# Kernel optimization log

Hardware: AMD Instinct MI355X
Metric: run time of the kernel (lower is better)

The kernel has to match this reference:

```python
import jax, jax.numpy as jnp
import numpy as np

S, B, D, H, DH = 2048, 2, 512, 8, 64
SCALE = 1.0 / DH ** 0.5
EPS = 1e-5
LN_EPS = 1e-5


def setup_inputs() -> dict:
    key = jax.random.key(0)
    k1, k2, k3, k4 = jax.random.split(key, 4)
    h = jax.random.normal(k1, (S, B, D), dtype=jnp.float32)
    # causal mask, True = masked out, shape [qlen, klen, 1] (dim==3 branch)
    attn_mask = jnp.triu(jnp.ones((S, S), dtype=bool), k=1)[:, :, None]
    Wq = jax.random.normal(k2, (D, H * DH), dtype=jnp.float32) * 0.02
    Wkv = jax.random.normal(k3, (D, 2 * H * DH), dtype=jnp.float32) * 0.02
    Wo = jax.random.normal(k4, (H * DH, D), dtype=jnp.float32) * 0.02
    gamma = jnp.ones((D,), dtype=jnp.float32)
    beta = jnp.zeros((D,), dtype=jnp.float32)
    return {"h": h, "Wq": Wq, "Wkv": Wkv, "Wo": Wo,
            "gamma": gamma, "beta": beta, "attn_mask": attn_mask}


def _layer_norm(x, gamma, beta):
    mu = jnp.mean(x, axis=-1, keepdims=True)
    var = jnp.mean(jnp.square(x - mu), axis=-1, keepdims=True)
    return (x - mu) * jax.lax.rsqrt(var + LN_EPS) * gamma + beta


def reference(h, Wq, Wkv, Wo, gamma, beta, attn_mask):
    # mems=None, pre_lnorm=False, dropout=dropatt=0 (eval)
    c = h
    head_q = (h @ Wq).reshape(S, B, H, DH)
    kv = (c @ Wkv)
    head_k, head_v = jnp.split(kv, 2, axis=-1)
    head_k = head_k.reshape(S, B, H, DH)
    head_v = head_v.reshape(S, B, H, DH)
    # elu(x) + 1 feature map
    head_q = jax.nn.elu(head_q) + 1.0
    head_k = jax.nn.elu(head_k) + 1.0
    # quadratic score matrix [i, j, b, n]
    attn_score = jnp.einsum('ibnd,jbnd->ijbn', head_q, head_k) * SCALE
    # dim==3 mask: [qlen, klen, 1] -> [qlen, klen, 1, 1], fill with 0
    attn_score = jnp.where(attn_mask[:, :, :, None], 0.0, attn_score)
    # sum-normalize over key axis (dim 1 = j)
    denominator = jnp.sum(attn_score, axis=1, keepdims=True) + EPS
    attn_prob = attn_score / denominator
    attn_vec = jnp.einsum('ijbn,jbnd->ibnd', attn_prob, head_v)
    attn_vec = attn_vec.reshape(S, B, H * DH)
    attn_out = attn_vec @ Wo
    # post-lnorm residual
    return _layer_norm(h + attn_out, gamma, beta)
```

## Files before the change

kernel.cpp:

```cpp
#include <hip/hip_runtime.h>
#include <hip/hip_bf16.h>
#include <math.h>

#define SCALE 0.125f
#define EPS 1e-5f
#define LN_EPS 1e-5f

typedef short short8 __attribute__((ext_vector_type(8)));
typedef float floatx4 __attribute__((ext_vector_type(4)));
typedef unsigned short us;

__device__ __forceinline__ float elu1(float x) { return x > 0.f ? x + 1.f : __expf(x); }
__device__ __forceinline__ us f2bf(float f) {
    __hip_bfloat16 b = __float2bfloat16(f);
    return __builtin_bit_cast(us, b);
}
__device__ __forceinline__ void gload_lds16(const void* g, void* lds) {
    __builtin_amdgcn_global_load_lds(
        (const __attribute__((address_space(1))) unsigned int*)g,
        (__attribute__((address_space(3))) unsigned int*)lds, 16, 0, 0);
}
__device__ __forceinline__ floatx4 mfma_bf16(short8 a, short8 b, floatx4 c) {
    return __builtin_amdgcn_mfma_f32_16x16x32_bf16(a, b, c, 0, 0, 0);
}

__global__ __launch_bounds__(256)
void pack_kernel(const float* __restrict__ h, const float* __restrict__ Wq,
                 const float* __restrict__ Wkv, const float* __restrict__ Wo,
                 us* __restrict__ hB, us* __restrict__ WqkvT, us* __restrict__ WoT,
                 us* __restrict__ VTg) {
    const int bid = blockIdx.x, tid = threadIdx.x;
    if (bid < 2048) {
        int idx = bid * 1024 + tid * 4;
        float4 v = *(const float4*)(h + idx);
        ushort4 o;
        o.x = f2bf(v.x); o.y = f2bf(v.y); o.z = f2bf(v.z); o.w = f2bf(v.w);
        *(ushort4*)(hB + idx) = o;
        return;
    }
    if (bid < 2304) {
        __shared__ us T[64][72];
        const float* src; int ld, n0s, k0; us* dst;
        if (bid < 2240) {
            int t2 = bid - 2048;
            int nt = t2 % 24, kt = t2 / 24;
            int n0 = nt * 64; k0 = kt * 64;
            if (n0 < 512) { src = Wq; ld = 512; n0s = n0; }
            else          { src = Wkv; ld = 1024; n0s = n0 - 512; }
            dst = WqkvT + (size_t)n0 * 512;
        } else {
            int t2 = bid - 2240;
            int nt = t2 & 7, kt = t2 >> 3;
            src = Wo; ld = 512; n0s = nt * 64; k0 = kt * 64;
            dst = WoT + (size_t)(nt * 64) * 512;
        }
        {
            int k = tid >> 2, cs = (tid & 3) * 16;
            const float* p = src + (size_t)(k0 + k) * ld + n0s + cs;
#pragma unroll
            for (int q = 0; q < 4; ++q) {
                float4 v = *(const float4*)(p + q * 4);
                T[k][cs + q * 4 + 0] = f2bf(v.x);
                T[k][cs + q * 4 + 1] = f2bf(v.y);
                T[k][cs + q * 4 + 2] = f2bf(v.z);
                T[k][cs + q * 4 + 3] = f2bf(v.w);
            }
        }
        __syncthreads();
        {
            int n = tid >> 2, ks = (tid & 3) * 16;
            __align__(16) us tmp[16];
#pragma unroll
            for (int j = 0; j < 16; ++j) tmp[j] = T[ks + j][n];
            us* po = dst + (size_t)n * 512 + k0 + ks;
            *(uint4*)(po) = *(uint4*)(tmp);
            *(uint4*)(po + 8) = *(uint4*)(tmp + 8);
        }
        return;
    }
    {
        int e = (bid - 2304) * 1024 + tid * 4;
        int chain = e >> 11, s = e & 2047;
        ushort4 o; o.x = 0x3f80; o.y = 0x3f80; o.z = 0x3f80; o.w = 0x3f80;
        *(ushort4*)(VTg + ((size_t)(chain * 80 + 64)) * 2048 + s) = o;
    }
}

__global__ __launch_bounds__(256)
void qkv_gemm(const us* __restrict__ A, const us* __restrict__ BT,
              us* __restrict__ Qg, us* __restrict__ Kg, us* __restrict__ VTg) {
    __shared__ __align__(16) us As[2][64 * 32];
    __shared__ __align__(16) us Bs[2][128 * 32];
    const int tid = threadIdx.x;
    const int w = tid >> 6, l = tid & 63;
    const int l15 = l & 15, l4 = l >> 4;
    const int bx = blockIdx.x;
    const int m0 = blockIdx.y * 64, n0 = bx * 128;
    const int wm = (w >> 1) * 32, wn = (w & 1) * 64;
    floatx4 acc[2][4];
#pragma unroll
    for (int i = 0; i < 2; ++i)
#pragma unroll
        for (int j = 0; j < 4; ++j)
#pragma unroll
            for (int e = 0; e < 4; ++e) acc[i][j][e] = 0.f;

    auto STAGE = [&](int buf, int kt) {
        {
            int row = w * 16 + (l >> 2);
            int g = (l & 3) ^ (row & 3);
            gload_lds16(A + (size_t)(m0 + row) * 512 + kt + g * 8, &As[buf][w * 512]);
        }
#pragma unroll
        for (int r = 0; r < 2; ++r) {
            int slot = r * 4 + w;
            int row = slot * 16 + (l >> 2);
            int g = (l & 3) ^ (row & 3);
            gload_lds16(BT + (size_t)(n0 + row) * 512 + kt + g * 8, &Bs[buf][slot * 512]);
        }
    };

    STAGE(0, 0);
    __syncthreads();
    for (int t = 0; t < 16; ++t) {
        int cur = t & 1;
        if (t < 15) STAGE(cur ^ 1, (t + 1) * 32);
        short8 a[2], b[4];
#pragma unroll
        for (int mi = 0; mi < 2; ++mi) {
            int row = wm + mi * 16 + l15;
            int p = l4 ^ (row & 3);
            a[mi] = *(const short8*)(&As[cur][row * 32 + p * 8]);
        }
#pragma unroll
        for (int ni = 0; ni < 4; ++ni) {
            int row = wn + ni * 16 + l15;
            int p = l4 ^ (row & 3);
            b[ni] = *(const short8*)(&Bs[cur][row * 32 + p * 8]);
        }
#pragma unroll
        for (int mi = 0; mi < 2; ++mi)
#pragma unroll
            for (int ni = 0; ni < 4; ++ni)
                acc[mi][ni] = mfma_bf16(a[mi], b[ni], acc[mi][ni]);
        __syncthreads();
    }
    const int region = bx >> 2;
    const int cb = (bx & 3) * 128;
    if (region < 2) {
        us* outp = region == 0 ? Qg : Kg;
#pragma unroll
        for (int mi = 0; mi < 2; ++mi)
#pragma unroll
            for (int ni = 0; ni < 4; ++ni)
#pragma unroll
                for (int r = 0; r < 4; ++r) {
                    int row = m0 + wm + mi * 16 + l4 * 4 + r;
                    int col = cb + wn + ni * 16 + l15;
                    outp[(size_t)row * 512 + col] = f2bf(elu1(acc[mi][ni][r]));
                }
    } else {
        const int hh = (bx & 3) * 2 + (w & 1);
#pragma unroll
        for (int mi = 0; mi < 2; ++mi) {
            int row0 = m0 + wm + mi * 16 + l4 * 4;
            int s0 = row0 >> 1;
#pragma unroll
            for (int ni = 0; ni < 4; ++ni) {
                int d = ni * 16 + l15;
#pragma unroll
                for (int b = 0; b < 2; ++b) {
                    unsigned int pk = (unsigned int)f2bf(acc[mi][ni][b]) |
                                      ((unsigned int)f2bf(acc[mi][ni][2 + b]) << 16);
                    *(unsigned int*)(VTg + ((size_t)((b * 8 + hh) * 80 + d)) * 2048 + s0) = pk;
                }
            }
        }
    }
}

__global__ __launch_bounds__(256)
void chunk_kv_kernel(const us* __restrict__ Kg, const us* __restrict__ VTg,
                     float* __restrict__ KVc) {
    __shared__ __align__(16) us VT_l[80 * 64];
    __shared__ __align__(16) us KT_l[64 * 72];
    const int c = blockIdx.x, chain = blockIdx.y;
    const int b = chain >> 3, hh = chain & 7;
    const int tid = threadIdx.x;
    const int w = tid >> 6, l = tid & 63;
    const int lrow = l >> 3, lg = l & 7;
#pragma unroll
    for (int r = 0; r < 3; ++r) {
        int slot = r * 4 + w;
        if (slot < 10) {
            int row = slot * 8 + lrow;
            int g = lg ^ (row & 7);
            gload_lds16(VTg + (size_t)(chain * 80 + row) * 2048 + c * 64 + g * 8,
                        VT_l + slot * 512);
        }
    }
#pragma unroll
    for (int gi = 0; gi < 2; ++gi) {
        int g = w + gi * 4;
        __align__(16) us kk[8];
#pragma unroll
        for (int e = 0; e < 8; ++e)
            kk[e] = Kg[(size_t)((c * 64 + g * 8 + e) * 2 + b) * 512 + hh * 64 + l];
        *(uint4*)(KT_l + l * 72 + g * 8) = *(uint4*)kk;
    }
    __syncthreads();
    const int l15 = l & 15, l4 = l >> 4;
    short8 af[5][2], bfr[2];
#pragma unroll
    for (int mi = 0; mi < 5; ++mi) {
        int row = mi * 16 + l15;
        int p = l4 ^ (row & 7);
        af[mi][0] = *(const short8*)(VT_l + row * 64 + p * 8);
        af[mi][1] = *(const short8*)(VT_l + row * 64 + (p ^ 4) * 8);
    }
    {
        int row = w * 16 + l15;
        bfr[0] = *(const short8*)(KT_l + row * 72 + l4 * 8);
        bfr[1] = *(const short8*)(KT_l + row * 72 + 32 + l4 * 8);
    }
    float* out = KVc + (size_t)(chain * 32 + c) * 4608;
#pragma unroll
    for (int mi = 0; mi < 5; ++mi) {
        floatx4 a = {0.f, 0.f, 0.f, 0.f};
        a = mfma_bf16(af[mi][0], bfr[0], a);
        a = mfma_bf16(af[mi][1], bfr[1], a);
#pragma unroll
        for (int r = 0; r < 4; ++r) {
            int row = mi * 16 + l4 * 4 + r;
            if (row < 65) out[row * 64 + w * 16 + l15] = a[r];
        }
    }
}

__global__ __launch_bounds__(256)
void cumsum_kernel(const float* __restrict__ KVc, us* __restrict__ MTg) {
    const int chain = blockIdx.x, rg = blockIdx.y;
    const int row = rg * 4 + (threadIdx.x >> 6), col = threadIdx.x & 63;
    const float* in = KVc + (size_t)chain * 32 * 4608 + row * 64 + col;
    us* out = MTg + ((size_t)chain * 32 * 80 + row) * 64 + col;
    float acc = 0.f;
#pragma unroll 4
    for (int cc = 0; cc < 32; ++cc) {
        out[(size_t)cc * 5120] = f2bf(acc);
        acc += in[(size_t)cc * 4608];
    }
}

__global__ __launch_bounds__(256)
void attn_kernel(const us* __restrict__ Qg, const us* __restrict__ Kg,
                 const us* __restrict__ VTg, const us* __restrict__ MTg,
                 us* __restrict__ ATT) {
    __shared__ __align__(16) us Qs[64 * 64];
    __shared__ __align__(16) us Ks[64 * 64];
    __shared__ __align__(16) us Vs[80 * 64];
    __shared__ __align__(16) us Ms[80 * 64];
    __shared__ __align__(16) us Sl[64 * 64];
    const int c = blockIdx.x, chain = blockIdx.y;
    const int b = chain >> 3, hh = chain & 7;
    const int tid = threadIdx.x;
    const int w = tid >> 6, l = tid & 63;
    const int l15 = l & 15, l4 = l >> 4;
    const int lrow = l >> 3, lg = l & 7;

#pragma unroll
    for (int r = 0; r < 2; ++r) {
        int slot = r * 4 + w;
        int row = slot * 8 + lrow;
        int g = lg ^ (row & 7);
        size_t grow = (size_t)((c * 64 + row) * 2 + b) * 512 + hh * 64 + g * 8;
        gload_lds16(Qg + grow, Qs + slot * 512);
        gload_lds16(Kg + grow, Ks + slot * 512);
    }
#pragma unroll
    for (int i = 0; i < 5; ++i) {
        int p = w * 5 + i;
        int s = p < 10 ? p : p - 10;
        int row = s * 8 + lrow;
        int g = lg ^ (row & 7);
        if (p < 10)
            gload_lds16(VTg + (size_t)(chain * 80 + row) * 2048 + c * 64 + g * 8,
                        Vs + s * 512);
        else
            gload_lds16(MTg + ((size_t)(chain * 32 + c) * 80 + row) * 64 + g * 8,
                        Ms + s * 512);
    }
    asm volatile("s_waitcnt vmcnt(5)" ::: "memory");
    __builtin_amdgcn_sched_barrier(0);
    __builtin_amdgcn_s_barrier();

    short8 qf[2];
    {
        int row = w * 16 + l15, p = l4 ^ (row & 7);
        qf[0] = *(const short8*)(Qs + row * 64 + p * 8);
        qf[1] = *(const short8*)(Qs + row * 64 + (p ^ 4) * 8);
    }
    short8 kf[4][2];
#pragma unroll
    for (int ni = 0; ni < 4; ++ni) {
        int row = ni * 16 + l15, p = l4 ^ (row & 7);
        kf[ni][0] = *(const short8*)(Ks + row * 64 + p * 8);
        kf[ni][1] = *(const short8*)(Ks + row * 64 + (p ^ 4) * 8);
    }

    const int ibase = w * 16 + l4 * 4;
#pragma unroll
    for (int ni = 0; ni < 4; ++ni) {
        floatx4 s = {0.f, 0.f, 0.f, 0.f};
        s = mfma_bf16(qf[0], kf[ni][0], s);
        s = mfma_bf16(qf[1], kf[ni][1], s);
        int col = ni * 16 + l15;
#pragma unroll
        for (int r = 0; r < 4; ++r) {
            int i = ibase + r;
            float v = (col <= i) ? s[r] : 0.f;
            Sl[i * 64 + (((col >> 3) ^ (i & 7)) * 8) + (col & 7)] = f2bf(v);
        }
    }
    short8 sf[2];
    {
        int ir = w * 16 + l15;
        sf[0] = *(const short8*)(Sl + ir * 64 + ((l4 ^ (ir & 7)) * 8));
        sf[1] = *(const short8*)(Sl + ir * 64 + (((4 + l4) ^ (ir & 7)) * 8));
    }
    __syncthreads();

    short8 vf[5][2], mf[5][2];
#pragma unroll
    for (int ni = 0; ni < 5; ++ni) {
        int row = ni * 16 + l15, p = l4 ^ (row & 7);
        vf[ni][0] = *(const short8*)(Vs + row * 64 + p * 8);
        vf[ni][1] = *(const short8*)(Vs + row * 64 + (p ^ 4) * 8);
        mf[ni][0] = *(const short8*)(Ms + row * 64 + p * 8);
        mf[ni][1] = *(const short8*)(Ms + row * 64 + (p ^ 4) * 8);
    }

    floatx4 acc[5];
#pragma unroll
    for (int ni = 0; ni < 5; ++ni) {
        floatx4 a = {0.f, 0.f, 0.f, 0.f};
        a = mfma_bf16(sf[0], vf[ni][0], a);
        a = mfma_bf16(sf[1], vf[ni][1], a);
        a = mfma_bf16(qf[0], mf[ni][0], a);
        a = mfma_bf16(qf[1], mf[ni][1], a);
        acc[ni] = a;
    }

    float fac[4];
#pragma unroll
    for (int r = 0; r < 4; ++r) {
        float den = __shfl(acc[4][r], l & 48, 64);
        fac[r] = SCALE / (SCALE * den + EPS);
    }
#pragma unroll
    for (int ni = 0; ni < 4; ++ni)
#pragma unroll
        for (int r = 0; r < 4; ++r) {
            int i = ibase + r;
            ATT[((size_t)((c * 64 + i) * 2 + b)) * 512 + hh * 64 + ni * 16 + l15] =
                f2bf(acc[ni][r] * fac[r]);
        }
}

__global__ __launch_bounds__(256)
void wo_ln_kernel(const us* __restrict__ ATT, const us* __restrict__ WoT,
                  const float* __restrict__ h, const float* __restrict__ gamma,
                  const float* __restrict__ beta, float* __restrict__ out) {
    __shared__ __align__(16) us As[2][16 * 32];
    __shared__ __align__(16) us Bs[2][512 * 32];
    __shared__ float redS[4][16];
    __shared__ float redQ[4][16];
    __shared__ float mml[16], rsl[16];
    const int tid = threadIdx.x;
    const int w = tid >> 6, l = tid & 63;
    const int l15 = l & 15, l4 = l >> 4;
    const int m0 = blockIdx.x * 16, wn = w * 128;
    floatx4 acc[8];
#pragma unroll
    for (int j = 0; j < 8; ++j)
#pragma unroll
        for (int e = 0; e < 4; ++e) acc[j][e] = 0.f;

    auto STAGE = [&](int buf, int kt) {
#pragma unroll
        for (int r = 0; r < 8; ++r) {
            int slot = r * 4 + w;
            int row = slot * 16 + (l >> 2);
            int g = (l & 3) ^ (row & 3);
            gload_lds16(WoT + (size_t)row * 512 + kt + g * 8, &Bs[buf][slot * 512]);
        }
        if (w == 0) {
            int row = l >> 2;
            int g = (l & 3) ^ (row & 3);
            gload_lds16(ATT + (size_t)(m0 + row) * 512 + kt + g * 8, &As[buf][0]);
        }
    };

    STAGE(0, 0);
    __syncthreads();
    for (int t = 0; t < 16; ++t) {
        int cur = t & 1;
        if (t < 15) STAGE(cur ^ 1, (t + 1) * 32);
        short8 af, bf[8];
        {
            int row = l15, p = l4 ^ (row & 3);
            af = *(const short8*)(&As[cur][row * 32 + p * 8]);
        }
#pragma unroll
        for (int ni = 0; ni < 8; ++ni) {
            int row = wn + ni * 16 + l15, p = l4 ^ (row & 3);
            bf[ni] = *(const short8*)(&Bs[cur][row * 32 + p * 8]);
        }
#pragma unroll
        for (int ni = 0; ni < 8; ++ni)
            acc[ni] = mfma_bf16(af, bf[ni], acc[ni]);
        __syncthreads();
    }

#pragma unroll
    for (int r = 0; r < 4; ++r) {
        int row = l4 * 4 + r;
        const float* hrow = h + (size_t)(m0 + row) * 512 + wn + l15;
        float s = 0.f, q = 0.f;
#pragma unroll
        for (int ni = 0; ni < 8; ++ni) {
            float x = acc[ni][r] + hrow[ni * 16];
            acc[ni][r] = x;
            s += x;
            q = fmaf(x, x, q);
        }
#pragma unroll
        for (int off = 1; off <= 8; off <<= 1) {
            s += __shfl_xor(s, off, 64);
            q += __shfl_xor(q, off, 64);
        }
        if (l15 == 0) { redS[w][row] = s; redQ[w][row] = q; }
    }
    __syncthreads();
    if (tid < 16) {
        float s = redS[0][tid] + redS[1][tid] + redS[2][tid] + redS[3][tid];
        float q = redQ[0][tid] + redQ[1][tid] + redQ[2][tid] + redQ[3][tid];
        float mean = s * (1.f / 512);
        float var = q * (1.f / 512) - mean * mean;
        mml[tid] = mean;
        rsl[tid] = rsqrtf(var + LN_EPS);
    }
    __syncthreads();
#pragma unroll
    for (int r = 0; r < 4; ++r) {
        int row = l4 * 4 + r;
        float mean = mml[row], rstd = rsl[row];
#pragma unroll
        for (int ni = 0; ni < 8; ++ni) {
            int col = wn + ni * 16 + l15;
            out[(size_t)(m0 + row) * 512 + col] =
                (acc[ni][r] - mean) * rstd * gamma[col] + beta[col];
        }
    }
}

extern "C" void kernel_launch(void* const* d_in, const int* in_sizes, int n_in,
                              void* d_out, int out_size, void* d_ws, size_t ws_size,
                              hipStream_t stream) {
    const float* h = (const float*)d_in[0];
    const float* Wq = (const float*)d_in[1];
    const float* Wkv = (const float*)d_in[2];
    const float* Wo = (const float*)d_in[3];
    const float* gamma = (const float*)d_in[4];
    const float* beta = (const float*)d_in[5];

    char* ws = (char*)d_ws;
    us* Qg      = (us*)(ws + 0);
    us* Kg      = (us*)(ws + 4194304);
    us* VTg     = (us*)(ws + 12582912);
    us* ATT     = (us*)(ws + 17825792);
    us* WoT     = (us*)(ws + 22020096);
    us* MTg     = (us*)(ws + 22544384);
    us* hB      = (us*)(ws + 27787264);
    us* WqkvT   = (us*)(ws + 31981568);
    float* KVc  = (float*)(ws + 33554432);

    dim3 blk(256);
    pack_kernel<<<2336, blk, 0, stream>>>(h, Wq, Wkv, Wo, hB, WqkvT, WoT, VTg);
    qkv_gemm<<<dim3(12, 64), blk, 0, stream>>>(hB, WqkvT, Qg, Kg, VTg);
    chunk_kv_kernel<<<dim3(32, 16), blk, 0, stream>>>(Kg, VTg, KVc);
    cumsum_kernel<<<dim3(16, 17), blk, 0, stream>>>(KVc, MTg);
    attn_kernel<<<dim3(32, 16), blk, 0, stream>>>(Qg, Kg, VTg, MTg, ATT);
    wo_ln_kernel<<<256, blk, 0, stream>>>(ATT, WoT, h, gamma, beta, (float*)d_out);
}
```

Baseline: 132.7 us.

## Fuse per-chunk KV state computation into QKV GEMM epilogue with head-interleaved K/V tiles

```diff
diff --git a/kernel.cpp b/kernel.cpp
--- a/kernel.cpp
+++ b/kernel.cpp
@@ -44,10 +44,14 @@
         if (bid < 2240) {
             int t2 = bid - 2048;
             int nt = t2 % 24, kt = t2 / 24;
-            int n0 = nt * 64; k0 = kt * 64;
-            if (n0 < 512) { src = Wq; ld = 512; n0s = n0; }
-            else          { src = Wkv; ld = 1024; n0s = n0 - 512; }
-            dst = WqkvT + (size_t)n0 * 512;
+            k0 = kt * 64;
+            if (nt < 8) { src = Wq; ld = 512; n0s = nt * 64; }
+            else {
+                int t = nt - 8, hh = t >> 1, half = t & 1;
+                src = Wkv; ld = 1024;
+                n0s = half ? 512 + hh * 64 : hh * 64;
+            }
+            dst = WqkvT + (size_t)(nt * 64) * 512;
         } else {
             int t2 = bid - 2240;
             int nt = t2 & 7, kt = t2 >> 3;
@@ -86,153 +90,162 @@
     }
 }
 
+union QkvSmem {
+    struct { us As[2][128 * 32]; us Bs[2][128 * 32]; } st;
+    us ET[128 * 130];
+};
+
 __global__ __launch_bounds__(256)
 void qkv_gemm(const us* __restrict__ A, const us* __restrict__ BT,
-              us* __restrict__ Qg, us* __restrict__ Kg, us* __restrict__ VTg) {
-    __shared__ __align__(16) us As[2][64 * 32];
-    __shared__ __align__(16) us Bs[2][128 * 32];
+              us* __restrict__ Qg, us* __restrict__ Kg, us* __restrict__ VTg,
+              float* __restrict__ KVc) {
+    __shared__ QkvSmem sm;
     const int tid = threadIdx.x;
     const int w = tid >> 6, l = tid & 63;
     const int l15 = l & 15, l4 = l >> 4;
-    const int bx = blockIdx.x;
-    const int m0 = blockIdx.y * 64, n0 = bx * 128;
-    const int wm = (w >> 1) * 32, wn = (w & 1) * 64;
-    floatx4 acc[2][4];
-#pragma unroll
-    for (int i = 0; i < 2; ++i)
+    const int ntile = blockIdx.x, c = blockIdx.y;
+    const int m0 = c * 128, n0 = ntile * 128;
+    const int wm = (w >> 1) * 64, wn = (w & 1) * 64;
+    floatx4 acc[4][4];
+#pragma unroll
+    for (int i = 0; i < 4; ++i)
 #pragma unroll
         for (int j = 0; j < 4; ++j)
 #pragma unroll
             for (int e = 0; e < 4; ++e) acc[i][j][e] = 0.f;
 
     auto STAGE = [&](int buf, int kt) {
-        {
-            int row = w * 16 + (l >> 2);
-            int g = (l & 3) ^ (row & 3);
-            gload_lds16(A + (size_t)(m0 + row) * 512 + kt + g * 8, &As[buf][w * 512]);
-        }
 #pragma unroll
         for (int r = 0; r < 2; ++r) {
-            int slot = r * 4 + w;
-            int row = slot * 16 + (l >> 2);
-            int g = (l & 3) ^ (row & 3);
-            gload_lds16(BT + (size_t)(n0 + row) * 512 + kt + g * 8, &Bs[buf][slot * 512]);
+            int slot = (r * 4 + w) * 64 + l;
+            int row = slot >> 2, part = slot & 3;
+            int g = part ^ (row & 3);
+            gload_lds16(A + (size_t)(m0 + row) * 512 + kt + g * 8,
+                        &sm.st.As[buf][(r * 4 + w) * 512]);
+            gload_lds16(BT + (size_t)(n0 + row) * 512 + kt + g * 8,
+                        &sm.st.Bs[buf][(r * 4 + w) * 512]);
         }
     };
-
     STAGE(0, 0);
     __syncthreads();
     for (int t = 0; t < 16; ++t) {
         int cur = t & 1;
         if (t < 15) STAGE(cur ^ 1, (t + 1) * 32);
-        short8 a[2], b[4];
-#pragma unroll
-        for (int mi = 0; mi < 2; ++mi) {
+        short8 a[4], b[4];
+#pragma unroll
+        for (int mi = 0; mi < 4; ++mi) {
             int row = wm + mi * 16 + l15;
             int p = l4 ^ (row & 3);
-            a[mi] = *(const short8*)(&As[cur][row * 32 + p * 8]);
+            a[mi] = *(const short8*)(&sm.st.As[cur][row * 32 + p * 8]);
         }
 #pragma unroll
         for (int ni = 0; ni < 4; ++ni) {
             int row = wn + ni * 16 + l15;
             int p = l4 ^ (row & 3);
-            b[ni] = *(const short8*)(&Bs[cur][row * 32 + p * 8]);
-        }
-#pragma unroll
-        for (int mi = 0; mi < 2; ++mi)
+            b[ni] = *(const short8*)(&sm.st.Bs[cur][row * 32 + p * 8]);
+        }
+#pragma unroll
+        for (int mi = 0; mi < 4; ++mi)
 #pragma unroll
             for (int ni = 0; ni < 4; ++ni)
                 acc[mi][ni] = mfma_bf16(a[mi], b[ni], acc[mi][ni]);
         __syncthreads();
     }
-    const int region = bx >> 2;
-    const int cb = (bx & 3) * 128;
-    if (region < 2) {
-        us* outp = region == 0 ? Qg : Kg;
-#pragma unroll
-        for (int mi = 0; mi < 2; ++mi)
+
+    if (ntile < 4) {
+        const int cb = ntile * 128;
+#pragma unroll
+        for (int mi = 0; mi < 4; ++mi)
 #pragma unroll
             for (int ni = 0; ni < 4; ++ni)
 #pragma unroll
                 for (int r = 0; r < 4; ++r) {
                     int row = m0 + wm + mi * 16 + l4 * 4 + r;
                     int col = cb + wn + ni * 16 + l15;
-                    outp[(size_t)row * 512 + col] = f2bf(elu1(acc[mi][ni][r]));
+                    Qg[(size_t)row * 512 + col] = f2bf(elu1(acc[mi][ni][r]));
+                }
+        return;
+    }
+
+    const int h = ntile - 4;
+    if ((w & 1) == 0) {
+#pragma unroll
+        for (int mi = 0; mi < 4; ++mi)
+#pragma unroll
+            for (int ni = 0; ni < 4; ++ni)
+#pragma unroll
+                for (int r = 0; r < 4; ++r) {
+                    int row = m0 + wm + mi * 16 + l4 * 4 + r;
+                    Kg[(size_t)row * 512 + h * 64 + ni * 16 + l15] =
+                        f2bf(elu1(acc[mi][ni][r]));
                 }
     } else {
-        const int hh = (bx & 3) * 2 + (w & 1);
-#pragma unroll
-        for (int mi = 0; mi < 2; ++mi) {
-            int row0 = m0 + wm + mi * 16 + l4 * 4;
-            int s0 = row0 >> 1;
+#pragma unroll
+        for (int mi = 0; mi < 4; ++mi) {
+            int base = m0 + wm + mi * 16 + l4 * 4;
+            int s0 = base >> 1;
 #pragma unroll
             for (int ni = 0; ni < 4; ++ni) {
-                int d = ni * 16 + l15;
-#pragma unroll
-                for (int b = 0; b < 2; ++b) {
-                    unsigned int pk = (unsigned int)f2bf(acc[mi][ni][b]) |
-                                      ((unsigned int)f2bf(acc[mi][ni][2 + b]) << 16);
-                    *(unsigned int*)(VTg + ((size_t)((b * 8 + hh) * 80 + d)) * 2048 + s0) = pk;
-                }
+                int dd = ni * 16 + l15;
+                unsigned int pk0 = (unsigned int)f2bf(acc[mi][ni][0]) |
+                                   ((unsigned int)f2bf(acc[mi][ni][2]) << 16);
+                unsigned int pk1 = (unsigned int)f2bf(acc[mi][ni][1]) |
+                                   ((unsigned int)f2bf(acc[mi][ni][3]) << 16);
+                *(unsigned int*)(VTg + ((size_t)(h * 80 + dd)) * 2048 + s0) = pk0;
+                *(unsigned int*)(VTg + ((size_t)((8 + h) * 80 + dd)) * 2048 + s0) = pk1;
             }
         }
     }
-}
-
-__global__ __launch_bounds__(256)
-void chunk_kv_kernel(const us* __restrict__ Kg, const us* __restrict__ VTg,
-                     float* __restrict__ KVc) {
-    __shared__ __align__(16) us VT_l[80 * 64];
-    __shared__ __align__(16) us KT_l[64 * 72];
-    const int c = blockIdx.x, chain = blockIdx.y;
-    const int b = chain >> 3, hh = chain & 7;
-    const int tid = threadIdx.x;
-    const int w = tid >> 6, l = tid & 63;
-    const int lrow = l >> 3, lg = l & 7;
-#pragma unroll
-    for (int r = 0; r < 3; ++r) {
-        int slot = r * 4 + w;
-        if (slot < 10) {
-            int row = slot * 8 + lrow;
-            int g = lg ^ (row & 7);
-            gload_lds16(VTg + (size_t)(chain * 80 + row) * 2048 + c * 64 + g * 8,
-                        VT_l + slot * 512);
-        }
-    }
-#pragma unroll
-    for (int gi = 0; gi < 2; ++gi) {
-        int g = w + gi * 4;
-        __align__(16) us kk[8];
-#pragma unroll
-        for (int e = 0; e < 8; ++e)
-            kk[e] = Kg[(size_t)((c * 64 + g * 8 + e) * 2 + b) * 512 + hh * 64 + l];
-        *(uint4*)(KT_l + l * 72 + g * 8) = *(uint4*)kk;
+
+#pragma unroll
+    for (int mi = 0; mi < 4; ++mi) {
+        int row0 = wm + mi * 16 + l4 * 4;
+        int s0 = row0 >> 1;
+#pragma unroll
+        for (int ni = 0; ni < 4; ++ni) {
+            int d = wn + ni * 16 + l15;
+            float v0 = acc[mi][ni][0], v1 = acc[mi][ni][1];
+            float v2 = acc[mi][ni][2], v3 = acc[mi][ni][3];
+            if (d < 64) { v0 = elu1(v0); v1 = elu1(v1); v2 = elu1(v2); v3 = elu1(v3); }
+            unsigned int w0 = (unsigned int)f2bf(v0) | ((unsigned int)f2bf(v2) << 16);
+            unsigned int w1 = (unsigned int)f2bf(v1) | ((unsigned int)f2bf(v3) << 16);
+            *(unsigned int*)(sm.ET + d * 130 + s0) = w0;
+            *(unsigned int*)(sm.ET + d * 130 + 64 + s0) = w1;
+        }
     }
     __syncthreads();
-    const int l15 = l & 15, l4 = l >> 4;
-    short8 af[5][2], bfr[2];
-#pragma unroll
-    for (int mi = 0; mi < 5; ++mi) {
-        int row = mi * 16 + l15;
-        int p = l4 ^ (row & 7);
-        af[mi][0] = *(const short8*)(VT_l + row * 64 + p * 8);
-        af[mi][1] = *(const short8*)(VT_l + row * 64 + (p ^ 4) * 8);
-    }
-    {
-        int row = w * 16 + l15;
-        bfr[0] = *(const short8*)(KT_l + row * 72 + l4 * 8);
-        bfr[1] = *(const short8*)(KT_l + row * 72 + 32 + l4 * 8);
-    }
-    float* out = KVc + (size_t)(chain * 32 + c) * 4608;
-#pragma unroll
-    for (int mi = 0; mi < 5; ++mi) {
-        floatx4 a = {0.f, 0.f, 0.f, 0.f};
-        a = mfma_bf16(af[mi][0], bfr[0], a);
-        a = mfma_bf16(af[mi][1], bfr[1], a);
-#pragma unroll
-        for (int r = 0; r < 4; ++r) {
-            int row = mi * 16 + l4 * 4 + r;
-            if (row < 65) out[row * 64 + w * 16 + l15] = a[r];
+
+    short8 ones8, zero8;
+#pragma unroll
+    for (int e = 0; e < 8; ++e) { ones8[e] = (short)0x3f80; zero8[e] = 0; }
+#pragma unroll 1
+    for (int b = 0; b < 2; ++b) {
+        const int off = b * 64;
+        short8 af[5][2], bfr[2];
+#pragma unroll
+        for (int mi = 0; mi < 4; ++mi) {
+            int dv = mi * 16 + l15;
+            af[mi][0] = *(const short8*)(sm.ET + (64 + dv) * 130 + off + l4 * 8);
+            af[mi][1] = *(const short8*)(sm.ET + (64 + dv) * 130 + off + 32 + l4 * 8);
+        }
+        af[4][0] = (l15 == 0) ? ones8 : zero8;
+        af[4][1] = af[4][0];
+        {
+            int dk = w * 16 + l15;
+            bfr[0] = *(const short8*)(sm.ET + dk * 130 + off + l4 * 8);
+            bfr[1] = *(const short8*)(sm.ET + dk * 130 + off + 32 + l4 * 8);
+        }
+        float* outkv = KVc + (size_t)((b * 8 + h) * 32 + c) * 4608;
+#pragma unroll
+        for (int mi = 0; mi < 5; ++mi) {
+            floatx4 a = {0.f, 0.f, 0.f, 0.f};
+            a = mfma_bf16(af[mi][0], bfr[0], a);
+            a = mfma_bf16(af[mi][1], bfr[1], a);
+#pragma unroll
+            for (int r = 0; r < 4; ++r) {
+                int row = mi * 16 + l4 * 4 + r;
+                if (row < 65) outkv[row * 64 + w * 16 + l15] = a[r];
+            }
         }
     }
 }
@@ -306,7 +319,6 @@
         kf[ni][0] = *(const short8*)(Ks + row * 64 + p * 8);
         kf[ni][1] = *(const short8*)(Ks + row * 64 + (p ^ 4) * 8);
     }
-
     const int ibase = w * 16 + l4 * 4;
 #pragma unroll
     for (int ni = 0; ni < 4; ++ni) {
@@ -338,7 +350,6 @@
         mf[ni][0] = *(const short8*)(Ms + row * 64 + p * 8);
         mf[ni][1] = *(const short8*)(Ms + row * 64 + (p ^ 4) * 8);
     }
-
     floatx4 acc[5];
 #pragma unroll
     for (int ni = 0; ni < 5; ++ni) {
@@ -349,7 +360,6 @@
         a = mfma_bf16(qf[1], mf[ni][1], a);
         acc[ni] = a;
     }
-
     float fac[4];
 #pragma unroll
     for (int r = 0; r < 4; ++r) {
@@ -486,8 +496,7 @@
 
     dim3 blk(256);
     pack_kernel<<<2336, blk, 0, stream>>>(h, Wq, Wkv, Wo, hB, WqkvT, WoT, VTg);
-    qkv_gemm<<<dim3(12, 64), blk, 0, stream>>>(hB, WqkvT, Qg, Kg, VTg);
-    chunk_kv_kernel<<<dim3(32, 16), blk, 0, stream>>>(Kg, VTg, KVc);
+    qkv_gemm<<<dim3(12, 32), blk, 0, stream>>>(hB, WqkvT, Qg, Kg, VTg, KVc);
     cumsum_kernel<<<dim3(16, 17), blk, 0, stream>>>(KVc, MTg);
     attn_kernel<<<dim3(32, 16), blk, 0, stream>>>(Qg, Kg, VTg, MTg, ATT);
     wo_ln_kernel<<<256, blk, 0, stream>>>(ATT, WoT, h, gamma, beta, (float*)d_out);
```

Result: no change. 135.2 us (+1.9%).
